# Kernel optimization log

Measured on AMD Instinct MI355X. Metric: run time of the kernel, lower is better.

## Reference

```python
import jax, jax.numpy as jnp
import numpy as np

MAX_ITERS = 50
EPS_NORM = 1e-8
EPS_SEP = -1e-6


def setup_inputs() -> dict:
    key = jax.random.key(0)
    k1, k2 = jax.random.split(key)
    pointcloud = jax.random.normal(k1, (200000, 3), dtype=jnp.float32)
    targets = jax.random.normal(k2, (256, 3), dtype=jnp.float32)
    return {"pointcloud": pointcloud, "targets": targets}


def reference(pointcloud, targets):
    # pointcloud: [N, d], targets: [M, d]
    N = pointcloud.shape[0]
    M = targets.shape[0]
    p2 = jnp.sum(pointcloud * pointcloud, axis=1)  # [N]
    t2 = jnp.sum(targets * targets, axis=1)        # [M]

    def step(mask, _):
        # squared euclidean distances [M, N] (argmin identical to cdist argmin)
        d2 = t2[:, None] + p2[None, :] - 2.0 * (targets @ pointcloud.T)
        d2 = jnp.where(mask, d2, jnp.inf)
        closest_idx = jnp.argmin(d2, axis=1)           # [M]
        closest_points = pointcloud[closest_idx]       # [M, d]
        a = closest_points - targets
        a = a / (jnp.linalg.norm(a, axis=1, keepdims=True) + EPS_NORM)
        b = jnp.sum(a * closest_points, axis=1)        # [M]
        dot = a @ pointcloud.T - b[:, None]            # [M, N]
        separated = dot >= EPS_SEP
        mask = mask & ~separated
        return mask, (a, b)

    mask0 = jnp.ones((M, N), dtype=bool)
    _, (a_stack, b_stack) = jax.lax.scan(step, mask0, None, length=MAX_ITERS)
    return a_stack, b_stack  # [MAX_ITERS, M, d], [MAX_ITERS, M]
```

## Files before the change

### kernel.cpp

```cpp
#include <hip/hip_runtime.h>
#include <stdint.h>
#include <math.h>

#pragma clang fp contract(off)

#define BLOCK 1024
#define NW (BLOCK / 64)
#define PT 8
#define PB 4
#define MAX_ITERS 50
#define SOLO_CAP 2048
#define NBINS 4096
#define EPS_NORM 1e-8f
#define EPS_SEP (-1e-6f)

__device__ __forceinline__ int bin_of(float x, float y, float z) {
    int cx = (int)floorf((x + 3.5f) * (16.0f / 7.0f));
    int cy = (int)floorf((y + 3.5f) * (16.0f / 7.0f));
    int cz = (int)floorf((z + 3.5f) * (16.0f / 7.0f));
    cx = cx < 0 ? 0 : (cx > 15 ? 15 : cx);
    cy = cy < 0 ? 0 : (cy > 15 ? 15 : cy);
    cz = cz < 0 ? 0 : (cz > 15 ? 15 : cz);
    int code = 0;
    #pragma unroll
    for (int b = 0; b < 4; ++b) {
        code |= ((cx >> b) & 1) << (3 * b);
        code |= ((cy >> b) & 1) << (3 * b + 1);
        code |= ((cz >> b) & 1) << (3 * b + 2);
    }
    return code;
}

__global__ void zero_bins(int* __restrict__ binCnt) {
    const int i = blockIdx.x * blockDim.x + threadIdx.x;
    if (i < NBINS) binCnt[i] = 0;
}

__global__ void hist_bins(const float* __restrict__ pc, int* __restrict__ binCnt,
                          int N) {
    const int i = blockIdx.x * blockDim.x + threadIdx.x;
    if (i < N)
        atomicAdd(&binCnt[bin_of(pc[3*i+0], pc[3*i+1], pc[3*i+2])], 1);
}

__global__ void scan_bins(const int* __restrict__ binCnt,
                          int* __restrict__ binCur) {
    __shared__ int wsum[16];
    const int t = threadIdx.x, lane = t & 63, wv = t >> 6;
    const int v0 = binCnt[4*t+0], v1 = binCnt[4*t+1],
              v2 = binCnt[4*t+2], v3 = binCnt[4*t+3];
    const int s = v0 + v1 + v2 + v3;
    int incl = s;
    #pragma unroll
    for (int off = 1; off < 64; off <<= 1) {
        int o = __shfl_up(incl, off, 64);
        if (lane >= off) incl += o;
    }
    if (lane == 63) wsum[wv] = incl;
    __syncthreads();
    if (t == 0) {
        int acc = 0;
        for (int w = 0; w < 16; ++w) { int x = wsum[w]; wsum[w] = acc; acc += x; }
    }
    __syncthreads();
    const int excl = incl - s + wsum[wv];
    binCur[4*t+0] = excl;
    binCur[4*t+1] = excl + v0;
    binCur[4*t+2] = excl + v0 + v1;
    binCur[4*t+3] = excl + v0 + v1 + v2;
}

__global__ void scatter_bins(const float* __restrict__ pc,
                             float4* __restrict__ pk,
                             int* __restrict__ binCur, int N) {
    const int i = blockIdx.x * blockDim.x + threadIdx.x;
    if (i < N) {
        const float x = pc[3*i+0], y = pc[3*i+1], z = pc[3*i+2];
        const int pos = atomicAdd(&binCur[bin_of(x, y, z)], 1);
        float4 v; v.x = x; v.y = y; v.z = z; v.w = __int_as_float(i);
        pk[pos] = v;
    }
}

__global__ void pack_identity(const float* __restrict__ pc,
                              float4* __restrict__ pk, int N) {
    const int i = blockIdx.x * blockDim.x + threadIdx.x;
    if (i < N) {
        float4 v; v.x = pc[3*i+0]; v.y = pc[3*i+1]; v.z = pc[3*i+2];
        v.w = __int_as_float(i);
        pk[i] = v;
    }
}

template <bool PK>
__global__ __launch_bounds__(BLOCK) void convex_plane_kernel(
    const float* __restrict__ pc, const float4* __restrict__ pk,
    const float* __restrict__ tg,
    float* __restrict__ out, int N, int M, int CAP, int stepsA)
{
    extern __shared__ uint32_t smem[];
    const int tid  = threadIdx.x;
    const int lane = tid & 63;
    const int wv   = tid >> 6;
    const int m    = blockIdx.x;

    const int maskW = stepsA * (PT * BLOCK / 32);
    uint32_t* mask  = smem;
    int*      list  = (int*)(smem + maskW);
    float*    red_d = (float*)(list + CAP);
    int*      red_i = (int*)(red_d + NW);
    int*      cw    = red_i + NW;
    int*      bcast = cw + NW;
    int*      cnt   = bcast + 2;
    int*      chk   = cnt + 1;

    const float tx = tg[3*m+0], ty = tg[3*m+1], tz = tg[3*m+2];
    const float t2 = tx*tx + ty*ty + tz*tz;

    float* out_a = out;
    float* out_b = out + (size_t)MAX_ITERS * (size_t)M * 3;

    auto finish = [&](float dmin, int imin, int mycnt, bool cntFromCursor) -> int2 {
        #pragma unroll
        for (int off = 32; off > 0; off >>= 1) {
            float od = __shfl_down(dmin, off, 64);
            int   oi = __shfl_down(imin, off, 64);
            int   oc = __shfl_down(mycnt, off, 64);
            if (od < dmin || (od == dmin && oi < imin)) { dmin = od; imin = oi; }
            mycnt += oc;
        }
        if (lane == 0) { red_d[wv] = dmin; red_i[wv] = imin; cw[wv] = mycnt; }
        __syncthreads();
        if (wv == 0) {
            float bd = (lane < NW) ? red_d[lane] : INFINITY;
            int   bi = (lane < NW) ? red_i[lane] : 0;
            int   c  = (lane < NW) ? cw[lane]    : 0;
            #pragma unroll
            for (int off = 8; off > 0; off >>= 1) {
                float od = __shfl_down(bd, off, 64);
                int   oi = __shfl_down(bi, off, 64);
                int   oc = __shfl_down(c,  off, 64);
                if (od < bd || (od == bd && oi < bi)) { bd = od; bi = oi; }
                c += oc;
            }
            if (lane == 0) { bcast[0] = bi; bcast[1] = cntFromCursor ? cnt[0] : c; }
        }
        __syncthreads();
        int2 r; r.x = bcast[0]; r.y = bcast[1];
        return r;
    };

    auto scanA = [&](int mode, bool build,
                     float ax, float ay, float az, float b) -> int2 {
        if (tid == 0) cnt[0] = 0;
        __syncthreads();
        float dmin = INFINITY;
        int   imin = 0;
        int   mycnt = 0;
        for (int s = 0; s < stepsA; ++s) {
            const int cid = s * NW + wv;
            if (mode == 2 && chk[cid] == 0) continue;
            const int pbase = s * (PT * BLOCK) + wv * (PT * 64) + lane;
            const int wwb   = s * (PT * BLOCK / 32) + wv * (PT * 2);
            uint32_t livem = 0;
            if (mode == 2) {
                #pragma unroll
                for (int j = 0; j < PT; ++j) {
                    uint32_t w = mask[wwb + j * 2 + (lane >> 5)];
                    livem |= ((w >> (lane & 31)) & 1u) << j;
                }
            } else {
                #pragma unroll
                for (int j = 0; j < PT; ++j)
                    if (pbase + j * 64 < N) livem |= (1u << j);
            }
            float px[PT], py[PT], pz[PT]; int ov[PT];
            if constexpr (PK) {
                #pragma unroll
                for (int j = 0; j < PT; ++j) {
                    int ip = pbase + j * 64;
                    ip = ip < N ? ip : N - 1;
                    const float4 v = pk[ip];
                    px[j] = v.x; py[j] = v.y; pz[j] = v.z;
                    ov[j] = __float_as_int(v.w);
                }
            } else {
                #pragma unroll
                for (int j = 0; j < PT; ++j) {
                    int ip = pbase + j * 64;
                    ip = ip < N ? ip : N - 1;
                    const float* p = pc + 3 * (size_t)ip;
                    px[j] = p[0]; py[j] = p[1]; pz[j] = p[2];
                    ov[j] = ip;
                }
            }
            uint32_t keepm = 0;
            #pragma unroll
            for (int j = 0; j < PT; ++j) {
                if ((livem >> j) & 1u) {
                    bool keep;
                    if (mode == 0) keep = true;
                    else {
                        float dt = ax*px[j] + ay*py[j] + az*pz[j] - b;
                        keep = (dt < EPS_SEP);
                    }
                    if (keep) {
                        keepm |= (1u << j);
                        float p2 = px[j]*px[j] + py[j]*py[j] + pz[j]*pz[j];
                        float tp = tx*px[j] + ty*py[j] + tz*pz[j];
                        float d2 = t2 + p2 - 2.0f*tp;
                        if (d2 < dmin || (d2 == dmin && ov[j] < imin)) {
                            dmin = d2; imin = ov[j];
                        }
                    }
                }
            }
            mycnt += (int)__popc(keepm);
            if (mode != 0) {
                #pragma unroll
                for (int j = 0; j < PT; ++j) {
                    unsigned long long bal = __ballot(((keepm >> j) & 1u) != 0u);
                    if (lane == 0)       mask[wwb + j*2]     = (uint32_t)bal;
                    else if (lane == 32) mask[wwb + j*2 + 1] = (uint32_t)(bal >> 32);
                }
                int wsumc = (int)__popc(keepm);
                #pragma unroll
                for (int off = 32; off > 0; off >>= 1)
                    wsumc += __shfl_down(wsumc, off, 64);
                if (lane == 0) chk[cid] = wsumc;
            }
            if (build) {
                int c = (int)__popc(keepm);
                int incl = c;
                #pragma unroll
                for (int off = 1; off < 64; off <<= 1) {
                    int o = __shfl_up(incl, off, 64);
                    if (lane >= off) incl += o;
                }
                const int excl = incl - c;
                const int tot  = __shfl(incl, 63, 64);
                int wb = 0;
                if (lane == 0) wb = atomicAdd(cnt, tot);
                wb = __shfl(wb, 0, 64);
                int pos = wb + excl;
                #pragma unroll
                for (int j = 0; j < PT; ++j) {
                    if ((keepm >> j) & 1u) {
                        if (pos < CAP) list[pos] = pbase + j * 64;
                        ++pos;
                    }
                }
            }
        }
        return finish(dmin, imin, mycnt, false);
    };

    auto scanB = [&](int count, float ax, float ay, float az, float b) -> int2 {
        if (tid == 0) cnt[0] = 0;
        __syncthreads();
        float dmin = INFINITY;
        int   imin = 0;
        const int per = BLOCK * PB;
        const int bsteps = (count + per - 1) / per;
        for (int s = 0; s < bsteps; ++s) {
            int jv[PB]; float xv[PB], yv[PB], zv[PB]; int ov[PB]; float d2v[PB];
            #pragma unroll
            for (int q = 0; q < PB; ++q) {
                int e = s * per + q * BLOCK + tid;
                e = e < count ? e : count - 1;
                jv[q] = list[e];
            }
            #pragma unroll
            for (int q = 0; q < PB; ++q) {
                if constexpr (PK) {
                    const float4 v = pk[jv[q]];
                    xv[q] = v.x; yv[q] = v.y; zv[q] = v.z;
                    ov[q] = __float_as_int(v.w);
                } else {
                    const float* p = pc + 3 * (size_t)jv[q];
                    xv[q] = p[0]; yv[q] = p[1]; zv[q] = p[2];
                    ov[q] = jv[q];
                }
            }
            uint32_t keepm = 0;
            #pragma unroll
            for (int q = 0; q < PB; ++q) {
                const int e = s * per + q * BLOCK + tid;
                if (e < count) {
                    float dt = ax*xv[q] + ay*yv[q] + az*zv[q] - b;
                    if (dt < EPS_SEP) {
                        keepm |= (1u << q);
                        float p2 = xv[q]*xv[q] + yv[q]*yv[q] + zv[q]*zv[q];
                        float tp = tx*xv[q] + ty*yv[q] + tz*zv[q];
                        d2v[q] = t2 + p2 - 2.0f*tp;
                    }
                }
            }
            __syncthreads();
            int c = (int)__popc(keepm);
            int incl = c;
            #pragma unroll
            for (int off = 1; off < 64; off <<= 1) {
                int o = __shfl_up(incl, off, 64);
                if (lane >= off) incl += o;
            }
            const int excl = incl - c;
            const int tot  = __shfl(incl, 63, 64);
            int wb = 0;
            if (lane == 0) wb = atomicAdd(cnt, tot);
            wb = __shfl(wb, 0, 64);
            int pos = wb + excl;
            #pragma unroll
            for (int q = 0; q < PB; ++q) {
                if ((keepm >> q) & 1u) {
                    list[pos] = jv[q];
                    if (d2v[q] < dmin || (d2v[q] == dmin && ov[q] < imin)) {
                        dmin = d2v[q]; imin = ov[q];
                    }
                    ++pos;
                }
            }
        }
        __syncthreads();
        return finish(dmin, imin, 0, true);
    };

    bool comp = false;
    int2 rc = scanA(0, false, 0.f, 0.f, 0.f, 0.f);
    int idx = rc.x, count = rc.y;

    for (int k = 0; k < MAX_ITERS; ++k) {
        if (comp && count <= SOLO_CAP) {
            float* lx = (float*)(list + SOLO_CAP);
            float* ly = lx + SOLO_CAP;
            float* lz = ly + SOLO_CAP;
            for (int e = tid; e < count; e += BLOCK) {
                if constexpr (PK) {
                    const float4 v = pk[list[e]];
                    lx[e] = v.x; ly[e] = v.y; lz[e] = v.z;
                    list[e] = __float_as_int(v.w);
                } else {
                    const float* p = pc + 3 * (size_t)list[e];
                    lx[e] = p[0]; ly[e] = p[1]; lz[e] = p[2];
                }
            }
            __syncthreads();
            if (wv != 0) return;
            for (; k < MAX_ITERS; ++k) {
                const float* cp = pc + 3 * (size_t)idx;
                const float cx = cp[0], cy = cp[1], cz = cp[2];
                const float vx = cx - tx, vy = cy - ty, vz = cz - tz;
                const float nrm = sqrtf(vx*vx + vy*vy + vz*vz);
                const float den = nrm + EPS_NORM;
                const float ax = vx / den, ay = vy / den, az = vz / den;
                const float b  = ax*cx + ay*cy + az*cz;
                if (count == 0) {
                    for (int q = lane; q < MAX_ITERS - k; q += 64) {
                        const int kk = k + q;
                        const size_t oa = ((size_t)kk * M + m) * 3;
                        out_a[oa+0] = ax; out_a[oa+1] = ay; out_a[oa+2] = az;
                        out_b[(size_t)kk * M + m] = b;
                    }
                    return;
                }
                if (lane == 0) {
                    const size_t oa = ((size_t)k * M + m) * 3;
                    out_a[oa+0] = ax; out_a[oa+1] = ay; out_a[oa+2] = az;
                    out_b[(size_t)k * M + m] = b;
                }
                if (k + 1 < MAX_ITERS) {
                    float dmin = INFINITY; int imin = 0; int wcur = 0;
                    for (int e0 = 0; e0 < count; e0 += 64) {
                        const int e = e0 + lane;
                        bool keep = false; int j = 0;
                        float d2v = 0.f, px = 0.f, py = 0.f, pz = 0.f;
                        if (e < count) {
                            j = list[e];
                            px = lx[e]; py = ly[e]; pz = lz[e];
                            float dt = ax*px + ay*py + az*pz - b;
                            if (dt < EPS_SEP) {
                                keep = true;
                                float p2 = px*px + py*py + pz*pz;
                                float tp = tx*px + ty*py + tz*pz;
                                d2v = t2 + p2 - 2.0f*tp;
                            }
                        }
                        unsigned long long bal = __ballot(keep);
                        int pos = wcur + (int)__popcll(bal & ((1ull << lane) - 1ull));
                        if (keep) {
                            list[pos] = j;
                            lx[pos] = px; ly[pos] = py; lz[pos] = pz;
                            if (d2v < dmin || (d2v == dmin && j < imin)) {
                                dmin = d2v; imin = j;
                            }
                        }
                        wcur += (int)__popcll(bal);
                    }
                    #pragma unroll
                    for (int off = 32; off > 0; off >>= 1) {
                        float od = __shfl_down(dmin, off, 64);
                        int   oi = __shfl_down(imin, off, 64);
                        if (od < dmin || (od == dmin && oi < imin)) { dmin = od; imin = oi; }
                    }
                    idx = __shfl(imin, 0, 64);
                    count = wcur;
                }
            }
            return;
        }

        const float* cp = pc + 3 * (size_t)idx;
        const float cx = cp[0], cy = cp[1], cz = cp[2];
        const float vx = cx - tx, vy = cy - ty, vz = cz - tz;
        const float nrm = sqrtf(vx*vx + vy*vy + vz*vz);
        const float den = nrm + EPS_NORM;
        const float ax = vx / den, ay = vy / den, az = vz / den;
        const float b  = ax*cx + ay*cy + az*cz;

        if (count == 0) {
            for (int q = tid; q < MAX_ITERS - k; q += BLOCK) {
                const int kk = k + q;
                const size_t oa = ((size_t)kk * M + m) * 3;
                out_a[oa+0] = ax; out_a[oa+1] = ay; out_a[oa+2] = az;
                out_b[(size_t)kk * M + m] = b;
            }
            return;
        }
        if (tid == 0) {
            const size_t oa = ((size_t)k * M + m) * 3;
            out_a[oa+0] = ax; out_a[oa+1] = ay; out_a[oa+2] = az;
            out_b[(size_t)k * M + m] = b;
        }
        if (k + 1 < MAX_ITERS) {
            if (comp) {
                rc = scanB(count, ax, ay, az, b);
            } else {
                const bool build = (count <= (5 * CAP) / 2);
                rc = scanA(k == 0 ? 1 : 2, build, ax, ay, az, b);
                if (build && rc.y <= CAP) comp = true;
            }
            idx = rc.x; count = rc.y;
        }
    }
}

extern "C" void kernel_launch(void* const* d_in, const int* in_sizes, int n_in,
                              void* d_out, int out_size, void* d_ws, size_t ws_size,
                              hipStream_t stream) {
    const float* pc = (const float*)d_in[0];
    const float* tg = (const float*)d_in[1];
    float* out = (float*)d_out;
    const int N = in_sizes[0] / 3;
    const int M = in_sizes[1] / 3;
    const int stepsA = (N + BLOCK * PT - 1) / (BLOCK * PT);
    const size_t maskB  = (size_t)stepsA * (PT * BLOCK / 32) * sizeof(uint32_t);
    const size_t fixedB = NW * (2 * sizeof(int) + sizeof(float)) + 3 * sizeof(int)
                        + (size_t)stepsA * NW * sizeof(int);
    const size_t pkB    = (size_t)N * sizeof(float4);
    const size_t binB   = 2 * (size_t)NBINS * sizeof(int);

    int wsmode = 0;
    if (d_ws && ws_size >= pkB + binB) wsmode = 2;
    else if (d_ws && ws_size >= pkB)   wsmode = 1;
    float4* pk     = (float4*)d_ws;
    int*    binCnt = (int*)((char*)d_ws + pkB);
    int*    binCur = binCnt + NBINS;

    int CAP = 32768;
    size_t smem = maskB + (size_t)CAP * sizeof(int) + fixedB;
    const void* fn = (wsmode >= 1) ? (const void*)convex_plane_kernel<true>
                                   : (const void*)convex_plane_kernel<false>;
    if (hipFuncSetAttribute(fn, hipFuncAttributeMaxDynamicSharedMemorySize,
                            (int)smem) != hipSuccess) {
        CAP = 8192;
        smem = maskB + (size_t)CAP * sizeof(int) + fixedB;
    }
    if (wsmode == 2) {
        const int tpb = 256;
        zero_bins<<<(NBINS + tpb - 1) / tpb, tpb, 0, stream>>>(binCnt);
        hist_bins<<<(N + tpb - 1) / tpb, tpb, 0, stream>>>(pc, binCnt, N);
        scan_bins<<<1, 1024, 0, stream>>>(binCnt, binCur);
        scatter_bins<<<(N + tpb - 1) / tpb, tpb, 0, stream>>>(pc, pk, binCur, N);
        convex_plane_kernel<true><<<M, BLOCK, smem, stream>>>(
            pc, pk, tg, out, N, M, CAP, stepsA);
    } else if (wsmode == 1) {
        pack_identity<<<(N + 255) / 256, 256, 0, stream>>>(pc, pk, N);
        convex_plane_kernel<true><<<M, BLOCK, smem, stream>>>(
            pc, pk, tg, out, N, M, CAP, stepsA);
    } else {
        convex_plane_kernel<false><<<M, BLOCK, smem, stream>>>(
            pc, nullptr, tg, out, N, M, CAP, stepsA);
    }
}
```

Baseline: 576.7 us.

## Replace compaction list with per-chunk bounding boxes to skip separated chunks

Drops the large compacted index list and scanB pass. Each 512-point chunk now stores its bounding box, count and local argmin in shared memory, and each iteration tests the plane against the box. Chunks that lie fully on one side are either skipped untouched or cleared without loading their points. The histogram and scatter prep kernels now read float4 vectors, and a memset replaces the zero kernel. The box test relies on slack thresholds to stay conservative, and it drops the shared list capacity tuning, which frees LDS and may change occupancy.

```diff
diff --git a/kernel.cpp b/kernel.cpp
--- a/kernel.cpp
+++ b/kernel.cpp
@@ -5,14 +5,15 @@
 #pragma clang fp contract(off)
 
 #define BLOCK 1024
-#define NW (BLOCK / 64)
+#define NW 16
 #define PT 8
-#define PB 4
 #define MAX_ITERS 50
 #define SOLO_CAP 2048
 #define NBINS 4096
 #define EPS_NORM 1e-8f
 #define EPS_SEP (-1e-6f)
+#define SLACK_ABS 1e-3f
+#define SLACK_REL 1e-5f
 
 __device__ __forceinline__ int bin_of(float x, float y, float z) {
     int cx = (int)floorf((x + 3.5f) * (16.0f / 7.0f));
@@ -31,16 +32,21 @@
     return code;
 }
 
-__global__ void zero_bins(int* __restrict__ binCnt) {
-    const int i = blockIdx.x * blockDim.x + threadIdx.x;
-    if (i < NBINS) binCnt[i] = 0;
-}
-
 __global__ void hist_bins(const float* __restrict__ pc, int* __restrict__ binCnt,
                           int N) {
-    const int i = blockIdx.x * blockDim.x + threadIdx.x;
-    if (i < N)
-        atomicAdd(&binCnt[bin_of(pc[3*i+0], pc[3*i+1], pc[3*i+2])], 1);
+    const int t = blockIdx.x * blockDim.x + threadIdx.x;
+    const int base = t * 4;
+    if (base + 3 < N) {
+        const float4* p4 = (const float4*)pc;
+        const float4 a = p4[3*t+0], b = p4[3*t+1], c = p4[3*t+2];
+        atomicAdd(&binCnt[bin_of(a.x, a.y, a.z)], 1);
+        atomicAdd(&binCnt[bin_of(a.w, b.x, b.y)], 1);
+        atomicAdd(&binCnt[bin_of(b.z, b.w, c.x)], 1);
+        atomicAdd(&binCnt[bin_of(c.y, c.z, c.w)], 1);
+    } else {
+        for (int i = base; i < N; ++i)
+            atomicAdd(&binCnt[bin_of(pc[3*i], pc[3*i+1], pc[3*i+2])], 1);
+    }
 }
 
 __global__ void scan_bins(const int* __restrict__ binCnt,
@@ -73,12 +79,28 @@
 __global__ void scatter_bins(const float* __restrict__ pc,
                              float4* __restrict__ pk,
                              int* __restrict__ binCur, int N) {
-    const int i = blockIdx.x * blockDim.x + threadIdx.x;
-    if (i < N) {
-        const float x = pc[3*i+0], y = pc[3*i+1], z = pc[3*i+2];
-        const int pos = atomicAdd(&binCur[bin_of(x, y, z)], 1);
-        float4 v; v.x = x; v.y = y; v.z = z; v.w = __int_as_float(i);
-        pk[pos] = v;
+    const int t = blockIdx.x * blockDim.x + threadIdx.x;
+    const int base = t * 4;
+    if (base + 3 < N) {
+        const float4* p4 = (const float4*)pc;
+        const float4 a = p4[3*t+0], b = p4[3*t+1], c = p4[3*t+2];
+        float x[4] = {a.x, a.w, b.z, c.y};
+        float y[4] = {a.y, b.x, b.w, c.z};
+        float z[4] = {a.z, b.y, c.x, c.w};
+        #pragma unroll
+        for (int q = 0; q < 4; ++q) {
+            const int pos = atomicAdd(&binCur[bin_of(x[q], y[q], z[q])], 1);
+            float4 v; v.x = x[q]; v.y = y[q]; v.z = z[q];
+            v.w = __int_as_float(base + q);
+            pk[pos] = v;
+        }
+    } else {
+        for (int i = base; i < N; ++i) {
+            const float xx = pc[3*i], yy = pc[3*i+1], zz = pc[3*i+2];
+            const int pos = atomicAdd(&binCur[bin_of(xx, yy, zz)], 1);
+            float4 v; v.x = xx; v.y = yy; v.z = zz; v.w = __int_as_float(i);
+            pk[pos] = v;
+        }
     }
 }
 
@@ -96,7 +118,7 @@
 __global__ __launch_bounds__(BLOCK) void convex_plane_kernel(
     const float* __restrict__ pc, const float4* __restrict__ pk,
     const float* __restrict__ tg,
-    float* __restrict__ out, int N, int M, int CAP, int stepsA)
+    float* __restrict__ out, int N, int M, int stepsA)
 {
     extern __shared__ uint32_t smem[];
     const int tid  = threadIdx.x;
@@ -104,15 +126,27 @@
     const int wv   = tid >> 6;
     const int m    = blockIdx.x;
 
+    const int NC    = stepsA * NW;
     const int maskW = stepsA * (PT * BLOCK / 32);
-    uint32_t* mask  = smem;
-    int*      list  = (int*)(smem + maskW);
-    float*    red_d = (float*)(list + CAP);
-    int*      red_i = (int*)(red_d + NW);
-    int*      cw    = red_i + NW;
-    int*      bcast = cw + NW;
-    int*      cnt   = bcast + 2;
-    int*      chk   = cnt + 1;
+    uint32_t* mask = smem;
+    float* mnx = (float*)(mask + maskW);
+    float* mny = mnx + NC;
+    float* mnz = mny + NC;
+    float* mxx = mnz + NC;
+    float* mxy = mxx + NC;
+    float* mxz = mxy + NC;
+    float* cdm = mxz + NC;
+    int*   cim = (int*)(cdm + NC);
+    int*   ccn = cim + NC;
+    float* red_d = (float*)(ccn + NC);
+    int*   red_i = (int*)(red_d + NW);
+    int*   cw    = red_i + NW;
+    int*   bcast = cw + NW;
+    int*   cnt   = bcast + 2;
+    int*   slist = cnt + 1;
+    float* lx = (float*)(slist + SOLO_CAP);
+    float* ly = lx + SOLO_CAP;
+    float* lz = ly + SOLO_CAP;
 
     const float tx = tg[3*m+0], ty = tg[3*m+1], tz = tg[3*m+2];
     const float t2 = tx*tx + ty*ty + tz*tz;
@@ -120,91 +154,164 @@
     float* out_a = out;
     float* out_b = out + (size_t)MAX_ITERS * (size_t)M * 3;
 
-    auto finish = [&](float dmin, int imin, int mycnt, bool cntFromCursor) -> int2 {
+    auto ld8 = [&](int pbase, float px[PT], float py[PT], float pz[PT],
+                   int ov[PT]) {
+        #pragma unroll
+        for (int j = 0; j < PT; ++j) {
+            int ip = pbase + j * 64;
+            ip = ip < N ? ip : N - 1;
+            if constexpr (PK) {
+                const float4 v = pk[ip];
+                px[j] = v.x; py[j] = v.y; pz[j] = v.z;
+                ov[j] = __float_as_int(v.w);
+            } else {
+                const float* p = pc + 3 * (size_t)ip;
+                px[j] = p[0]; py[j] = p[1]; pz[j] = p[2];
+                ov[j] = ip;
+            }
+        }
+    };
+
+    auto finish = [&]() -> int2 {
+        __syncthreads();
+        float bd = INFINITY; int bi = 0; int cs = 0;
+        for (int l = lane; l < stepsA; l += 64) {
+            const int c = wv + NW * l;
+            const float d = cdm[c]; const int i = cim[c];
+            if (d < bd || (d == bd && i < bi)) { bd = d; bi = i; }
+            cs += ccn[c];
+        }
+        #pragma unroll
+        for (int off = 32; off > 0; off >>= 1) {
+            float od = __shfl_down(bd, off, 64);
+            int   oi = __shfl_down(bi, off, 64);
+            int   oc = __shfl_down(cs, off, 64);
+            if (od < bd || (od == bd && oi < bi)) { bd = od; bi = oi; }
+            cs += oc;
+        }
+        if (lane == 0) { red_d[wv] = bd; red_i[wv] = bi; cw[wv] = cs; }
+        __syncthreads();
+        if (wv == 0) {
+            float d = (lane < NW) ? red_d[lane] : INFINITY;
+            int   i = (lane < NW) ? red_i[lane] : 0;
+            int   c = (lane < NW) ? cw[lane]    : 0;
+            #pragma unroll
+            for (int off = 8; off > 0; off >>= 1) {
+                float od = __shfl_down(d, off, 64);
+                int   oi = __shfl_down(i, off, 64);
+                int   oc = __shfl_down(c, off, 64);
+                if (od < d || (od == d && oi < i)) { d = od; i = oi; }
+                c += oc;
+            }
+            if (lane == 0) { bcast[0] = i; bcast[1] = c; }
+        }
+        __syncthreads();
+        int2 r; r.x = bcast[0]; r.y = bcast[1];
+        return r;
+    };
+
+    auto writeChunk = [&](int c, uint32_t keepm,
+                          float dmin, int imin,
+                          float px[PT], float py[PT], float pz[PT]) {
+        float nx = INFINITY, ny = INFINITY, nz = INFINITY;
+        float Xx = -INFINITY, Xy = -INFINITY, Xz = -INFINITY;
+        #pragma unroll
+        for (int j = 0; j < PT; ++j) {
+            if ((keepm >> j) & 1u) {
+                nx = fminf(nx, px[j]); ny = fminf(ny, py[j]); nz = fminf(nz, pz[j]);
+                Xx = fmaxf(Xx, px[j]); Xy = fmaxf(Xy, py[j]); Xz = fmaxf(Xz, pz[j]);
+            }
+        }
+        int cntl = (int)__popc(keepm);
         #pragma unroll
         for (int off = 32; off > 0; off >>= 1) {
             float od = __shfl_down(dmin, off, 64);
             int   oi = __shfl_down(imin, off, 64);
-            int   oc = __shfl_down(mycnt, off, 64);
             if (od < dmin || (od == dmin && oi < imin)) { dmin = od; imin = oi; }
-            mycnt += oc;
-        }
-        if (lane == 0) { red_d[wv] = dmin; red_i[wv] = imin; cw[wv] = mycnt; }
-        __syncthreads();
-        if (wv == 0) {
-            float bd = (lane < NW) ? red_d[lane] : INFINITY;
-            int   bi = (lane < NW) ? red_i[lane] : 0;
-            int   c  = (lane < NW) ? cw[lane]    : 0;
-            #pragma unroll
-            for (int off = 8; off > 0; off >>= 1) {
-                float od = __shfl_down(bd, off, 64);
-                int   oi = __shfl_down(bi, off, 64);
-                int   oc = __shfl_down(c,  off, 64);
-                if (od < bd || (od == bd && oi < bi)) { bd = od; bi = oi; }
-                c += oc;
-            }
-            if (lane == 0) { bcast[0] = bi; bcast[1] = cntFromCursor ? cnt[0] : c; }
-        }
-        __syncthreads();
-        int2 r; r.x = bcast[0]; r.y = bcast[1];
-        return r;
+            cntl += __shfl_down(cntl, off, 64);
+            nx = fminf(nx, __shfl_down(nx, off, 64));
+            ny = fminf(ny, __shfl_down(ny, off, 64));
+            nz = fminf(nz, __shfl_down(nz, off, 64));
+            Xx = fmaxf(Xx, __shfl_down(Xx, off, 64));
+            Xy = fmaxf(Xy, __shfl_down(Xy, off, 64));
+            Xz = fmaxf(Xz, __shfl_down(Xz, off, 64));
+        }
+        if (lane == 0) {
+            cdm[c] = dmin; cim[c] = imin; ccn[c] = cntl;
+            mnx[c] = nx; mny[c] = ny; mnz[c] = nz;
+            mxx[c] = Xx; mxy[c] = Xy; mxz[c] = Xz;
+        }
     };
 
-    auto scanA = [&](int mode, bool build,
-                     float ax, float ay, float az, float b) -> int2 {
-        if (tid == 0) cnt[0] = 0;
-        __syncthreads();
-        float dmin = INFINITY;
-        int   imin = 0;
-        int   mycnt = 0;
+    auto initScan = [&]() {
         for (int s = 0; s < stepsA; ++s) {
-            const int cid = s * NW + wv;
-            if (mode == 2 && chk[cid] == 0) continue;
+            const int c = s * NW + wv;
             const int pbase = s * (PT * BLOCK) + wv * (PT * 64) + lane;
             const int wwb   = s * (PT * BLOCK / 32) + wv * (PT * 2);
             uint32_t livem = 0;
-            if (mode == 2) {
-                #pragma unroll
-                for (int j = 0; j < PT; ++j) {
-                    uint32_t w = mask[wwb + j * 2 + (lane >> 5)];
-                    livem |= ((w >> (lane & 31)) & 1u) << j;
-                }
-            } else {
-                #pragma unroll
-                for (int j = 0; j < PT; ++j)
-                    if (pbase + j * 64 < N) livem |= (1u << j);
-            }
+            #pragma unroll
+            for (int j = 0; j < PT; ++j)
+                if (pbase + j * 64 < N) livem |= (1u << j);
             float px[PT], py[PT], pz[PT]; int ov[PT];
-            if constexpr (PK) {
-                #pragma unroll
-                for (int j = 0; j < PT; ++j) {
-                    int ip = pbase + j * 64;
-                    ip = ip < N ? ip : N - 1;
-                    const float4 v = pk[ip];
-                    px[j] = v.x; py[j] = v.y; pz[j] = v.z;
-                    ov[j] = __float_as_int(v.w);
-                }
-            } else {
-                #pragma unroll
-                for (int j = 0; j < PT; ++j) {
-                    int ip = pbase + j * 64;
-                    ip = ip < N ? ip : N - 1;
-                    const float* p = pc + 3 * (size_t)ip;
-                    px[j] = p[0]; py[j] = p[1]; pz[j] = p[2];
-                    ov[j] = ip;
-                }
-            }
-            uint32_t keepm = 0;
+            ld8(pbase, px, py, pz, ov);
+            float dmin = INFINITY; int imin = 0;
             #pragma unroll
             for (int j = 0; j < PT; ++j) {
                 if ((livem >> j) & 1u) {
-                    bool keep;
-                    if (mode == 0) keep = true;
-                    else {
-                        float dt = ax*px[j] + ay*py[j] + az*pz[j] - b;
-                        keep = (dt < EPS_SEP);
+                    float p2 = px[j]*px[j] + py[j]*py[j] + pz[j]*pz[j];
+                    float tp = tx*px[j] + ty*py[j] + tz*pz[j];
+                    float d2 = t2 + p2 - 2.0f*tp;
+                    if (d2 < dmin || (d2 == dmin && ov[j] < imin)) {
+                        dmin = d2; imin = ov[j];
                     }
-                    if (keep) {
+                }
+            }
+            #pragma unroll
+            for (int j = 0; j < PT; ++j) {
+                unsigned long long bal = __ballot(((livem >> j) & 1u) != 0u);
+                if (lane == 0)       mask[wwb + j*2]     = (uint32_t)bal;
+                else if (lane == 32) mask[wwb + j*2 + 1] = (uint32_t)(bal >> 32);
+            }
+            writeChunk(c, livem, dmin, imin, px, py, pz);
+        }
+    };
+
+    auto stepScan = [&](float ax, float ay, float az, float b) {
+        for (int s = 0; s < stepsA; ++s) {
+            const int c = s * NW + wv;
+            if (ccn[c] == 0) continue;
+            const float ubx = fmaxf(ax*mnx[c], ax*mxx[c]);
+            const float uby = fmaxf(ay*mny[c], ay*mxy[c]);
+            const float ubz = fmaxf(az*mnz[c], az*mxz[c]);
+            const float ub  = (ubx + uby + ubz) - b;
+            const float sl  = SLACK_ABS + SLACK_REL * (fabsf(ub) + fabsf(b));
+            if (ub < EPS_SEP - sl) continue;
+            const float lbx = fminf(ax*mnx[c], ax*mxx[c]);
+            const float lby = fminf(ay*mny[c], ay*mxy[c]);
+            const float lbz = fminf(az*mnz[c], az*mxz[c]);
+            const float lb  = (lbx + lby + lbz) - b;
+            const float sl2 = SLACK_ABS + SLACK_REL * (fabsf(lb) + fabsf(b));
+            if (lb >= EPS_SEP + sl2) {
+                if (lane == 0) { ccn[c] = 0; cdm[c] = INFINITY; }
+                continue;
+            }
+            const int pbase = s * (PT * BLOCK) + wv * (PT * 64) + lane;
+            const int wwb   = s * (PT * BLOCK / 32) + wv * (PT * 2);
+            uint32_t livem = 0;
+            #pragma unroll
+            for (int j = 0; j < PT; ++j) {
+                uint32_t w = mask[wwb + j * 2 + (lane >> 5)];
+                livem |= ((w >> (lane & 31)) & 1u) << j;
+            }
+            float px[PT], py[PT], pz[PT]; int ov[PT];
+            ld8(pbase, px, py, pz, ov);
+            uint32_t keepm = 0;
+            float dmin = INFINITY; int imin = 0;
+            #pragma unroll
+            for (int j = 0; j < PT; ++j) {
+                if ((livem >> j) & 1u) {
+                    float dt = ax*px[j] + ay*py[j] + az*pz[j] - b;
+                    if (dt < EPS_SEP) {
                         keepm |= (1u << j);
                         float p2 = px[j]*px[j] + py[j]*py[j] + pz[j]*pz[j];
                         float tp = tx*px[j] + ty*py[j] + tz*pz[j];
@@ -215,29 +322,45 @@
                     }
                 }
             }
-            mycnt += (int)__popc(keepm);
-            if (mode != 0) {
+            #pragma unroll
+            for (int j = 0; j < PT; ++j) {
+                unsigned long long bal = __ballot(((keepm >> j) & 1u) != 0u);
+                if (lane == 0)       mask[wwb + j*2]     = (uint32_t)bal;
+                else if (lane == 32) mask[wwb + j*2 + 1] = (uint32_t)(bal >> 32);
+            }
+            writeChunk(c, keepm, dmin, imin, px, py, pz);
+        }
+    };
+
+    initScan();
+    int2 rc = finish();
+    int idx = rc.x, count = rc.y;
+
+    for (int k = 0; k < MAX_ITERS; ++k) {
+        if (count <= SOLO_CAP && count > 0) {
+            if (tid == 0) cnt[0] = 0;
+            __syncthreads();
+            for (int s = 0; s < stepsA; ++s) {
+                const int c = s * NW + wv;
+                if (ccn[c] == 0) continue;
+                const int pbase = s * (PT * BLOCK) + wv * (PT * 64) + lane;
+                const int wwb   = s * (PT * BLOCK / 32) + wv * (PT * 2);
+                uint32_t livem = 0;
                 #pragma unroll
                 for (int j = 0; j < PT; ++j) {
-                    unsigned long long bal = __ballot(((keepm >> j) & 1u) != 0u);
-                    if (lane == 0)       mask[wwb + j*2]     = (uint32_t)bal;
-                    else if (lane == 32) mask[wwb + j*2 + 1] = (uint32_t)(bal >> 32);
-                }
-                int wsumc = (int)__popc(keepm);
-                #pragma unroll
-                for (int off = 32; off > 0; off >>= 1)
-                    wsumc += __shfl_down(wsumc, off, 64);
-                if (lane == 0) chk[cid] = wsumc;
-            }
-            if (build) {
-                int c = (int)__popc(keepm);
-                int incl = c;
+                    uint32_t w = mask[wwb + j * 2 + (lane >> 5)];
+                    livem |= ((w >> (lane & 31)) & 1u) << j;
+                }
+                float px[PT], py[PT], pz[PT]; int ov[PT];
+                ld8(pbase, px, py, pz, ov);
+                int cl = (int)__popc(livem);
+                int incl = cl;
                 #pragma unroll
                 for (int off = 1; off < 64; off <<= 1) {
                     int o = __shfl_up(incl, off, 64);
                     if (lane >= off) incl += o;
                 }
-                const int excl = incl - c;
+                const int excl = incl - cl;
                 const int tot  = __shfl(incl, 63, 64);
                 int wb = 0;
                 if (lane == 0) wb = atomicAdd(cnt, tot);
@@ -245,103 +368,11 @@
                 int pos = wb + excl;
                 #pragma unroll
                 for (int j = 0; j < PT; ++j) {
-                    if ((keepm >> j) & 1u) {
-                        if (pos < CAP) list[pos] = pbase + j * 64;
+                    if ((livem >> j) & 1u) {
+                        slist[pos] = ov[j];
+                        lx[pos] = px[j]; ly[pos] = py[j]; lz[pos] = pz[j];
                         ++pos;
                     }
-                }
-            }
-        }
-        return finish(dmin, imin, mycnt, false);
-    };
-
-    auto scanB = [&](int count, float ax, float ay, float az, float b) -> int2 {
-        if (tid == 0) cnt[0] = 0;
-        __syncthreads();
-        float dmin = INFINITY;
-        int   imin = 0;
-        const int per = BLOCK * PB;
-        const int bsteps = (count + per - 1) / per;
-        for (int s = 0; s < bsteps; ++s) {
-            int jv[PB]; float xv[PB], yv[PB], zv[PB]; int ov[PB]; float d2v[PB];
-            #pragma unroll
-            for (int q = 0; q < PB; ++q) {
-                int e = s * per + q * BLOCK + tid;
-                e = e < count ? e : count - 1;
-                jv[q] = list[e];
-            }
-            #pragma unroll
-            for (int q = 0; q < PB; ++q) {
-                if constexpr (PK) {
-                    const float4 v = pk[jv[q]];
-                    xv[q] = v.x; yv[q] = v.y; zv[q] = v.z;
-                    ov[q] = __float_as_int(v.w);
-                } else {
-                    const float* p = pc + 3 * (size_t)jv[q];
-                    xv[q] = p[0]; yv[q] = p[1]; zv[q] = p[2];
-                    ov[q] = jv[q];
-                }
-            }
-            uint32_t keepm = 0;
-            #pragma unroll
-            for (int q = 0; q < PB; ++q) {
-                const int e = s * per + q * BLOCK + tid;
-                if (e < count) {
-                    float dt = ax*xv[q] + ay*yv[q] + az*zv[q] - b;
-                    if (dt < EPS_SEP) {
-                        keepm |= (1u << q);
-                        float p2 = xv[q]*xv[q] + yv[q]*yv[q] + zv[q]*zv[q];
-                        float tp = tx*xv[q] + ty*yv[q] + tz*zv[q];
-                        d2v[q] = t2 + p2 - 2.0f*tp;
-                    }
-                }
-            }
-            __syncthreads();
-            int c = (int)__popc(keepm);
-            int incl = c;
-            #pragma unroll
-            for (int off = 1; off < 64; off <<= 1) {
-                int o = __shfl_up(incl, off, 64);
-                if (lane >= off) incl += o;
-            }
-            const int excl = incl - c;
-            const int tot  = __shfl(incl, 63, 64);
-            int wb = 0;
-            if (lane == 0) wb = atomicAdd(cnt, tot);
-            wb = __shfl(wb, 0, 64);
-            int pos = wb + excl;
-            #pragma unroll
-            for (int q = 0; q < PB; ++q) {
-                if ((keepm >> q) & 1u) {
-                    list[pos] = jv[q];
-                    if (d2v[q] < dmin || (d2v[q] == dmin && ov[q] < imin)) {
-                        dmin = d2v[q]; imin = ov[q];
-                    }
-                    ++pos;
-                }
-            }
-        }
-        __syncthreads();
-        return finish(dmin, imin, 0, true);
-    };
-
-    bool comp = false;
-    int2 rc = scanA(0, false, 0.f, 0.f, 0.f, 0.f);
-    int idx = rc.x, count = rc.y;
-
-    for (int k = 0; k < MAX_ITERS; ++k) {
-        if (comp && count <= SOLO_CAP) {
-            float* lx = (float*)(list + SOLO_CAP);
-            float* ly = lx + SOLO_CAP;
-            float* lz = ly + SOLO_CAP;
-            for (int e = tid; e < count; e += BLOCK) {
-                if constexpr (PK) {
-                    const float4 v = pk[list[e]];
-                    lx[e] = v.x; ly[e] = v.y; lz[e] = v.z;
-                    list[e] = __float_as_int(v.w);
-                } else {
-                    const float* p = pc + 3 * (size_t)list[e];
-                    lx[e] = p[0]; ly[e] = p[1]; lz[e] = p[2];
                 }
             }
             __syncthreads();
@@ -375,7 +406,7 @@
                         bool keep = false; int j = 0;
                         float d2v = 0.f, px = 0.f, py = 0.f, pz = 0.f;
                         if (e < count) {
-                            j = list[e];
+                            j = slist[e];
                             px = lx[e]; py = ly[e]; pz = lz[e];
                             float dt = ax*px + ay*py + az*pz - b;
                             if (dt < EPS_SEP) {
@@ -388,7 +419,7 @@
                         unsigned long long bal = __ballot(keep);
                         int pos = wcur + (int)__popcll(bal & ((1ull << lane) - 1ull));
                         if (keep) {
-                            list[pos] = j;
+                            slist[pos] = j;
                             lx[pos] = px; ly[pos] = py; lz[pos] = pz;
                             if (d2v < dmin || (d2v == dmin && j < imin)) {
                                 dmin = d2v; imin = j;
@@ -432,13 +463,8 @@
             out_b[(size_t)k * M + m] = b;
         }
         if (k + 1 < MAX_ITERS) {
-            if (comp) {
-                rc = scanB(count, ax, ay, az, b);
-            } else {
-                const bool build = (count <= (5 * CAP) / 2);
-                rc = scanA(k == 0 ? 1 : 2, build, ax, ay, az, b);
-                if (build && rc.y <= CAP) comp = true;
-            }
+            stepScan(ax, ay, az, b);
+            rc = finish();
             idx = rc.x; count = rc.y;
         }
     }
@@ -453,11 +479,13 @@
     const int N = in_sizes[0] / 3;
     const int M = in_sizes[1] / 3;
     const int stepsA = (N + BLOCK * PT - 1) / (BLOCK * PT);
-    const size_t maskB  = (size_t)stepsA * (PT * BLOCK / 32) * sizeof(uint32_t);
-    const size_t fixedB = NW * (2 * sizeof(int) + sizeof(float)) + 3 * sizeof(int)
-                        + (size_t)stepsA * NW * sizeof(int);
-    const size_t pkB    = (size_t)N * sizeof(float4);
-    const size_t binB   = 2 * (size_t)NBINS * sizeof(int);
+    const int NC     = stepsA * NW;
+    const int maskW  = stepsA * (PT * BLOCK / 32);
+    const size_t smemW = (size_t)maskW + 9u * NC + 3u * NW + 3u
+                       + 4u * SOLO_CAP;
+    const size_t smem  = smemW * sizeof(uint32_t);
+    const size_t pkB   = (size_t)N * sizeof(float4);
+    const size_t binB  = 2 * (size_t)NBINS * sizeof(int);
 
     int wsmode = 0;
     if (d_ws && ws_size >= pkB + binB) wsmode = 2;
@@ -466,29 +494,27 @@
     int*    binCnt = (int*)((char*)d_ws + pkB);
     int*    binCur = binCnt + NBINS;
 
-    int CAP = 32768;
-    size_t smem = maskB + (size_t)CAP * sizeof(int) + fixedB;
-    const void* fn = (wsmode >= 1) ? (const void*)convex_plane_kernel<true>
-                                   : (const void*)convex_plane_kernel<false>;
-    if (hipFuncSetAttribute(fn, hipFuncAttributeMaxDynamicSharedMemorySize,
-                            (int)smem) != hipSuccess) {
-        CAP = 8192;
-        smem = maskB + (size_t)CAP * sizeof(int) + fixedB;
-    }
+    hipFuncSetAttribute((const void*)convex_plane_kernel<true>,
+                        hipFuncAttributeMaxDynamicSharedMemorySize, (int)smem);
+    hipFuncSetAttribute((const void*)convex_plane_kernel<false>,
+                        hipFuncAttributeMaxDynamicSharedMemorySize, (int)smem);
+
     if (wsmode == 2) {
         const int tpb = 256;
-        zero_bins<<<(NBINS + tpb - 1) / tpb, tpb, 0, stream>>>(binCnt);
-        hist_bins<<<(N + tpb - 1) / tpb, tpb, 0, stream>>>(pc, binCnt, N);
+        const int vthreads = (N + 3) / 4;
+        hipMemsetAsync(binCnt, 0, NBINS * sizeof(int), stream);
+        hist_bins<<<(vthreads + tpb - 1) / tpb, tpb, 0, stream>>>(pc, binCnt, N);
         scan_bins<<<1, 1024, 0, stream>>>(binCnt, binCur);
-        scatter_bins<<<(N + tpb - 1) / tpb, tpb, 0, stream>>>(pc, pk, binCur, N);
+        scatter_bins<<<(vthreads + tpb - 1) / tpb, tpb, 0, stream>>>(pc, pk,
+                                                                     binCur, N);
         convex_plane_kernel<true><<<M, BLOCK, smem, stream>>>(
-            pc, pk, tg, out, N, M, CAP, stepsA);
+            pc, pk, tg, out, N, M, stepsA);
     } else if (wsmode == 1) {
         pack_identity<<<(N + 255) / 256, 256, 0, stream>>>(pc, pk, N);
         convex_plane_kernel<true><<<M, BLOCK, smem, stream>>>(
-            pc, pk, tg, out, N, M, CAP, stepsA);
+            pc, pk, tg, out, N, M, stepsA);
     } else {
         convex_plane_kernel<false><<<M, BLOCK, smem, stream>>>(
-            pc, nullptr, tg, out, N, M, CAP, stepsA);
-    }
-}
+            pc, nullptr, tg, out, N, M, stepsA);
+    }
+}
```

New measurement: 572.6 us. No clear change (-0.7%).
